# Performance work log

Measured on AMD Instinct MI355X. Metric: run time of the kernel, lower is better.

Reference implementation:

```python
import jax, jax.numpy as jnp
import numpy as np
import math

B, N, H, D = 2, 2048, 16, 64
NUM_BUCKETS, MAX_DIST = 32, 128
MODEL = H * D


def _rel_pos_bucket(rel, num_buckets, max_distance):
    # T5-style bucketing (bidirectional): half the buckets for sign, half log-spaced.
    nb = num_buckets // 2
    ret = (rel >= 0).astype(jnp.int32) * nb
    n = jnp.abs(rel)
    max_exact = nb // 2
    is_small = n < max_exact
    n_safe = jnp.maximum(n, 1).astype(jnp.float32)
    val_large = max_exact + (
        jnp.log(n_safe / max_exact) / math.log(max_distance / max_exact) * (nb - max_exact)
    ).astype(jnp.int32)
    val_large = jnp.minimum(val_large, nb - 1)
    return ret + jnp.where(is_small, n, val_large)


def _rel_pos_bias(rel_emb, n, m):
    q_pos = jnp.arange(m - n, m)
    k_pos = jnp.arange(m)
    rel = k_pos[None, :] - q_pos[:, None]            # [n, m]
    buckets = _rel_pos_bucket(rel, NUM_BUCKETS, MAX_DIST)
    bias = rel_emb[buckets]                          # [n, m, h]
    return bias.transpose(2, 0, 1)[None]             # [1, h, n, m]


def setup_inputs() -> dict:
    key = jax.random.key(0)
    ks = jax.random.split(key, 6)
    return {
        "q": jax.random.normal(ks[0], (B, N, MODEL), dtype=jnp.float32),
        "k": jax.random.normal(ks[1], (B, N, MODEL), dtype=jnp.float32),
        "v": jax.random.normal(ks[2], (B, N, MODEL), dtype=jnp.float32),
        "rel_emb": jax.random.normal(ks[3], (NUM_BUCKETS, H), dtype=jnp.float32) * 0.05,
        "w_out": jax.random.normal(ks[4], (MODEL, MODEL), dtype=jnp.float32) * (MODEL ** -0.5),
        "b_out": jax.random.normal(ks[5], (MODEL,), dtype=jnp.float32) * 0.02,
    }


def reference(q, k, v, rel_emb, w_out, b_out):
    b, n, _ = q.shape
    split = lambda x: x.reshape(b, n, H, D).transpose(0, 2, 1, 3)  # b h n d
    qh, kh, vh = split(q), split(k), split(v)
    sim = jnp.einsum('bhnd,bhmd->bhnm', qh, kh)
    sim = (sim + _rel_pos_bias(rel_emb, n, n)) * (D ** -0.5)  # note: scale AFTER bias, as in source
    attn = jax.nn.softmax(sim, axis=-1)
    out = jnp.einsum('bhnm,bhmd->bhnd', attn, vh)
    out = out.transpose(0, 2, 1, 3).reshape(b, n, H * D)
    return out @ w_out.T + b_out
```

## Files before the change

### kernel.cpp

```cpp
#include <hip/hip_runtime.h>

#define BB 2
#define NN 2048
#define HH 16
#define MODEL 1024
#define CSC 0.18033688011112042f

typedef short bf16x8 __attribute__((ext_vector_type(8)));
typedef float f32x4 __attribute__((ext_vector_type(4)));
typedef int i32x2 __attribute__((ext_vector_type(2)));

__device__ __forceinline__ unsigned short f2bf(float x) {
  unsigned int u = __builtin_bit_cast(unsigned int, x);
  u += 0x7fffu + ((u >> 16) & 1u);
  return (unsigned short)(u >> 16);
}

__device__ __forceinline__ unsigned int pack_bf2(float a, float b) {
  unsigned int ua = __builtin_bit_cast(unsigned int, a) + 0x8000u;
  unsigned int ub = __builtin_bit_cast(unsigned int, b) + 0x8000u;
  return __builtin_amdgcn_perm(ub, ua, 0x07060302u);
}

__device__ __forceinline__ float fast_exp2(float x) {
#if __has_builtin(__builtin_amdgcn_exp2f)
  return __builtin_amdgcn_exp2f(x);
#else
  return exp2f(x);
#endif
}

__device__ __forceinline__ f32x4 mfma16(bf16x8 a, bf16x8 b, f32x4 c) {
  return __builtin_amdgcn_mfma_f32_16x16x32_bf16(a, b, c, 0, 0, 0);
}

__device__ __forceinline__ void async_copy16(void* lds_base, const void* g) {
  __builtin_amdgcn_global_load_lds(
      (const __attribute__((address_space(1))) void*)g,
      (__attribute__((address_space(3))) void*)lds_base, 16, 0, 0);
}

__global__ void prep_kernel(const float* __restrict__ q, const float* __restrict__ k,
                            const float* __restrict__ w, const float* __restrict__ v,
                            const float* __restrict__ rel_emb,
                            unsigned short* __restrict__ qb, unsigned short* __restrict__ kb,
                            unsigned short* __restrict__ wb, unsigned short* __restrict__ vt,
                            float* __restrict__ biasTab) {
  __shared__ unsigned short tile[64][65];
  const int NQ4 = BB * NN * MODEL / 4;
  const int blk = blockIdx.x;
  if (blk < 9216) {
    int i = blk * 256 + threadIdx.x;
    const float* src;
    unsigned short* dst;
    int j = i;
    if (i < NQ4) {
      src = q; dst = qb;
    } else if (i < 2 * NQ4) {
      src = k; dst = kb; j = i - NQ4;
    } else {
      src = w; dst = wb; j = i - 2 * NQ4;
    }
    float4 f = reinterpret_cast<const float4*>(src)[j];
    ushort4 u;
    u.x = f2bf(f.x); u.y = f2bf(f.y); u.z = f2bf(f.z); u.w = f2bf(f.w);
    reinterpret_cast<ushort4*>(dst)[j] = u;
  } else if (blk < 10240) {
    const int blk2 = blk - 9216;
    const int n0 = (blk2 & 31) * 64;
    const int bh = blk2 >> 5;
    const int b = bh >> 4, h = bh & 15;
    const int c = threadIdx.x & 63;
    const int r = threadIdx.x >> 6;
#pragma unroll
    for (int i = 0; i < 16; ++i) {
      int nl = r * 16 + i;
      tile[c][nl] = f2bf(v[((long)(b * NN + n0 + nl)) * MODEL + h * 64 + c]);
    }
    __syncthreads();
#pragma unroll
    for (int i = 0; i < 16; ++i) {
      int d = r * 16 + i;
      vt[((long)(bh * 64 + d)) * NN + n0 + c] = tile[d][c];
    }
  } else {
    int idx = (blk - 10240) * 256 + threadIdx.x;
    if (idx >= 4095) return;
    int rel = idx - 2047;
    int nn = rel < 0 ? -rel : rel;
    int bucket;
    if (nn < 8) {
      bucket = nn;
    } else {
      float val = logf((float)nn * 0.125f) / logf(16.0f) * 8.0f;
      int vl = 8 + (int)val;
      if (vl > 15) vl = 15;
      bucket = vl;
    }
    if (rel >= 0) bucket += 16;
#pragma unroll
    for (int h = 0; h < 16; ++h)
      biasTab[h * 4095 + idx] = rel_emb[bucket * 16 + h] * CSC - 12.0f;
  }
}

__global__ __launch_bounds__(256, 2) void flash10(
    const unsigned short* __restrict__ qb, const unsigned short* __restrict__ kb,
    const unsigned short* __restrict__ vtb, const float* __restrict__ biasTab,
    unsigned short* __restrict__ attn) {
  __shared__ __align__(16) float obuf[4 * 64 * 68];
  __shared__ __align__(16) float scratch[512];

  const int i = blockIdx.x;
  const int bh = (i & 7) * 4 + ((i >> 3) >> 5);
  const int qt = (i >> 3) & 31;
  const int b = bh >> 4, h = bh & 15;
  const int q0 = qt * 64;
  const int tid = threadIdx.x, w = tid >> 6, lane = tid & 63;
  const int g = lane >> 4, c = lane & 15;

  const float* btab = biasTab + h * 4095 + 2047;
  for (int j = tid; j < 441; j += 256) scratch[j] = btab[j - 220];
  const float cPos = btab[200], cNeg = btab[-200];
  __syncthreads();

  bf16x8 qf0[4], qf1[4];
  const unsigned short* qbase = qb + ((long)(b * NN + q0)) * MODEL + h * 64;
#pragma unroll
  for (int nt = 0; nt < 4; ++nt) {
    const unsigned short* r = qbase + (16 * nt + c) * MODEL + 8 * g;
    qf0[nt] = *reinterpret_cast<const bf16x8*>(r);
    qf1[nt] = *reinterpret_cast<const bf16x8*>(r + 32);
  }

  const unsigned short* kbase = kb + ((long)b * NN) * MODEL + h * 64;
  const unsigned short* vbase = vtb + ((long)bh * 64) * NN;

  f32x4 o[4][4];
  float l_p[4] = {0.f, 0.f, 0.f, 0.f};
#pragma unroll
  for (int mt = 0; mt < 4; ++mt)
#pragma unroll
    for (int nt = 0; nt < 4; ++nt) o[mt][nt] = f32x4{0.f, 0.f, 0.f, 0.f};

  for (int it = 0; it < 8; ++it) {
    const int kt = w + 4 * it;
    bf16x8 kf0[4], kf1[4];
    const unsigned short* krow = kbase + (long)(kt * 64) * MODEL;
#pragma unroll
    for (int mt = 0; mt < 4; ++mt) {
      const unsigned short* r = krow + (16 * mt + c) * MODEL + 8 * g;
      kf0[mt] = *reinterpret_cast<const bf16x8*>(r);
      kf1[mt] = *reinterpret_cast<const bf16x8*>(r + 32);
    }
    bf16x8 vf0[4], vf1[4];
    const unsigned short* vrow = vbase + kt * 64;
#pragma unroll
    for (int mt = 0; mt < 4; ++mt) {
      const unsigned short* r = vrow + (long)(16 * mt + c) * NN + 8 * g;
      vf0[mt] = *reinterpret_cast<const bf16x8*>(r);
      vf1[mt] = *reinterpret_cast<const bf16x8*>(r + 32);
    }
    const int lo = kt * 64 - q0 - 63, hi = kt * 64 + 63 - q0;
    const bool sat = (lo >= 91 || hi <= -91);
    const float cb = (lo >= 91) ? cPos : cNeg;

#pragma unroll
    for (int nt = 0; nt < 4; ++nt) {
      f32x4 s[4];
#pragma unroll
      for (int mt = 0; mt < 4; ++mt) {
        s[mt] = mfma16(kf0[mt], qf0[nt], f32x4{0.f, 0.f, 0.f, 0.f});
        s[mt] = mfma16(kf1[mt], qf1[nt], s[mt]);
      }
      if (sat) {
#pragma unroll
        for (int mt = 0; mt < 4; ++mt)
#pragma unroll
          for (int rr = 0; rr < 4; ++rr) s[mt][rr] = s[mt][rr] * CSC + cb;
      } else {
        const int base = kt * 64 + 4 * g - q0 - 16 * nt - c + 220;
#pragma unroll
        for (int mt = 0; mt < 4; ++mt)
#pragma unroll
          for (int rr = 0; rr < 4; ++rr)
            s[mt][rr] = s[mt][rr] * CSC + scratch[base + 16 * mt + rr];
      }
      float sum = 0.f;
      unsigned int pk[4][2];
#pragma unroll
      for (int mt = 0; mt < 4; ++mt) {
        const float p0 = fast_exp2(s[mt][0]);
        const float p1 = fast_exp2(s[mt][1]);
        const float p2 = fast_exp2(s[mt][2]);
        const float p3 = fast_exp2(s[mt][3]);
        sum += (p0 + p1) + (p2 + p3);
        pk[mt][0] = pack_bf2(p0, p1);
        pk[mt][1] = pack_bf2(p2, p3);
      }
      l_p[nt] += sum;
      unsigned int d0, d1, d2, d3, d4, d5, d6, d7;
      {
        i32x2 x, y;
        x = __builtin_amdgcn_permlane32_swap((int)pk[0][0], (int)pk[1][0], false, false);
        y = __builtin_amdgcn_permlane16_swap(x[0], x[1], false, false);
        d0 = (unsigned int)y[0]; d2 = (unsigned int)y[1];
        x = __builtin_amdgcn_permlane32_swap((int)pk[0][1], (int)pk[1][1], false, false);
        y = __builtin_amdgcn_permlane16_swap(x[0], x[1], false, false);
        d1 = (unsigned int)y[0]; d3 = (unsigned int)y[1];
        x = __builtin_amdgcn_permlane32_swap((int)pk[2][0], (int)pk[3][0], false, false);
        y = __builtin_amdgcn_permlane16_swap(x[0], x[1], false, false);
        d4 = (unsigned int)y[0]; d6 = (unsigned int)y[1];
        x = __builtin_amdgcn_permlane32_swap((int)pk[2][1], (int)pk[3][1], false, false);
        y = __builtin_amdgcn_permlane16_swap(x[0], x[1], false, false);
        d5 = (unsigned int)y[0]; d7 = (unsigned int)y[1];
      }
      const bf16x8 pb0 = __builtin_bit_cast(bf16x8, uint4{d0, d1, d2, d3});
      const bf16x8 pb1 = __builtin_bit_cast(bf16x8, uint4{d4, d5, d6, d7});
#pragma unroll
      for (int mt = 0; mt < 4; ++mt) {
        o[mt][nt] = mfma16(vf0[mt], pb0, o[mt][nt]);
        o[mt][nt] = mfma16(vf1[mt], pb1, o[mt][nt]);
      }
    }
  }

  __syncthreads();
  float* ob = obuf + w * 64 * 68;
#pragma unroll
  for (int nt = 0; nt < 4; ++nt) {
    ob[(16 * nt + c) * 68 + 64 + g] = l_p[nt];
#pragma unroll
    for (int mt = 0; mt < 4; ++mt)
      *reinterpret_cast<f32x4*>(&ob[(16 * nt + c) * 68 + 16 * mt + 4 * g]) = o[mt][nt];
  }
  __syncthreads();

  const int qr = 16 * w + c;
  float l = 0.f;
#pragma unroll
  for (int u = 0; u < 4; ++u)
#pragma unroll
    for (int gg = 0; gg < 4; ++gg) l += obuf[(u * 64 + qr) * 68 + 64 + gg];
  const float inv = 1.f / l;

  float acc[16];
#pragma unroll
  for (int j = 0; j < 16; ++j) acc[j] = 0.f;
#pragma unroll
  for (int u = 0; u < 4; ++u) {
    const float* src = obuf + (u * 64 + qr) * 68;
    f32x4 r0 = *reinterpret_cast<const f32x4*>(&src[8 * g]);
    f32x4 r1 = *reinterpret_cast<const f32x4*>(&src[8 * g + 4]);
    f32x4 r2 = *reinterpret_cast<const f32x4*>(&src[32 + 8 * g]);
    f32x4 r3 = *reinterpret_cast<const f32x4*>(&src[32 + 8 * g + 4]);
#pragma unroll
    for (int j = 0; j < 4; ++j) {
      acc[j] += r0[j];
      acc[4 + j] += r1[j];
      acc[8 + j] += r2[j];
      acc[12 + j] += r3[j];
    }
  }
  unsigned int od[8];
#pragma unroll
  for (int t = 0; t < 8; ++t) od[t] = pack_bf2(acc[2 * t] * inv, acc[2 * t + 1] * inv);
  unsigned short* orow = attn + ((long)(b * NN + q0 + qr)) * MODEL + h * 64;
  *reinterpret_cast<uint4*>(orow + 8 * g) = uint4{od[0], od[1], od[2], od[3]};
  *reinterpret_cast<uint4*>(orow + 32 + 8 * g) = uint4{od[4], od[5], od[6], od[7]};
}

__global__ void proj_gemm_kernel(const unsigned short* __restrict__ A,
                                 const unsigned short* __restrict__ Bw,
                                 const float* __restrict__ bias,
                                 float* __restrict__ out) {
  __shared__ __align__(16) unsigned short At[2][128 * 64];
  __shared__ __align__(16) unsigned short Bt[2][64 * 64];
  int bm0 = blockIdx.x * 128, bn0 = blockIdx.y * 64;
  int tid = threadIdx.x, w = tid >> 6, lane = tid & 63;
  int g = lane >> 4, c = lane & 15;
  int m0 = (w & 1) * 64, n0 = (w >> 1) * 32;

  f32x4 acc[4][2];
#pragma unroll
  for (int mi = 0; mi < 4; ++mi)
#pragma unroll
    for (int nj = 0; nj < 2; ++nj) acc[mi][nj] = f32x4{0.f, 0.f, 0.f, 0.f};

  int rloc = lane >> 3, p = lane & 7;

  auto stage = [&](int buf, int kt) {
#pragma unroll
    for (int t = 0; t < 4; ++t) {
      int row = w * 32 + t * 8 + rloc;
      async_copy16(&At[buf][(w * 32 + t * 8) * 64],
                   A + (long)(bm0 + row) * 1024 + kt * 64 + (p ^ rloc) * 8);
    }
#pragma unroll
    for (int t = 0; t < 2; ++t) {
      int row = w * 16 + t * 8 + rloc;
      async_copy16(&Bt[buf][(w * 16 + t * 8) * 64],
                   Bw + (long)(bn0 + row) * 1024 + kt * 64 + (p ^ rloc) * 8);
    }
  };

  int cur = 0;
  stage(0, 0);
  for (int kt = 0; kt < 16; ++kt) {
    __syncthreads();
    if (kt < 15) stage(cur ^ 1, kt + 1);

    bf16x8 af0[4], af1[4], bf0[2], bf1[2];
#pragma unroll
    for (int mi = 0; mi < 4; ++mi) {
      int row = m0 + 16 * mi + c, sw = row & 7;
      af0[mi] = *reinterpret_cast<const bf16x8*>(&At[cur][row * 64 + (g ^ sw) * 8]);
      af1[mi] = *reinterpret_cast<const bf16x8*>(&At[cur][row * 64 + ((4 + g) ^ sw) * 8]);
    }
#pragma unroll
    for (int nj = 0; nj < 2; ++nj) {
      int row = n0 + 16 * nj + c, sw = row & 7;
      bf0[nj] = *reinterpret_cast<const bf16x8*>(&Bt[cur][row * 64 + (g ^ sw) * 8]);
      bf1[nj] = *reinterpret_cast<const bf16x8*>(&Bt[cur][row * 64 + ((4 + g) ^ sw) * 8]);
    }
#pragma unroll
    for (int mi = 0; mi < 4; ++mi)
#pragma unroll
      for (int nj = 0; nj < 2; ++nj) {
        acc[mi][nj] = mfma16(af0[mi], bf0[nj], acc[mi][nj]);
        acc[mi][nj] = mfma16(af1[mi], bf1[nj], acc[mi][nj]);
      }
    cur ^= 1;
  }

#pragma unroll
  for (int mi = 0; mi < 4; ++mi)
#pragma unroll
    for (int nj = 0; nj < 2; ++nj)
#pragma unroll
      for (int r = 0; r < 4; ++r) {
        int row = bm0 + m0 + mi * 16 + 4 * g + r;
        int col = bn0 + n0 + nj * 16 + c;
        out[(long)row * 1024 + col] = acc[mi][nj][r] + bias[col];
      }
}

extern "C" void kernel_launch(void* const* d_in, const int* in_sizes, int n_in,
                              void* d_out, int out_size, void* d_ws, size_t ws_size,
                              hipStream_t stream) {
  const float* q = (const float*)d_in[0];
  const float* k = (const float*)d_in[1];
  const float* v = (const float*)d_in[2];
  const float* rel_emb = (const float*)d_in[3];
  const float* w_out = (const float*)d_in[4];
  const float* b_out = (const float*)d_in[5];
  float* out = (float*)d_out;

  char* ws = (char*)d_ws;
  unsigned short* qb   = (unsigned short*)(ws);
  unsigned short* kb   = (unsigned short*)(ws + (8u << 20));
  unsigned short* vt   = (unsigned short*)(ws + (16u << 20));
  unsigned short* attn = (unsigned short*)(ws + (24u << 20));
  unsigned short* wb   = (unsigned short*)(ws + (32u << 20));
  float* biasTab       = (float*)(ws + (34u << 20));

  hipLaunchKernelGGL(prep_kernel, dim3(10257), dim3(256), 0, stream,
                     q, k, w_out, v, rel_emb, qb, kb, wb, vt, biasTab);
  hipLaunchKernelGGL(flash10, dim3(1024), dim3(256), 0, stream,
                     qb, kb, vt, biasTab, attn);
  hipLaunchKernelGGL(proj_gemm_kernel, dim3(32, 16), dim3(256), 0, stream,
                     attn, wb, b_out, out);
}
```

Before: 190.5 us.

## Fuse Q conversion into attention, double-buffer K loads, raise MFMA priority

Q is no longer converted to bf16 in the prep kernel. The attention kernel now reads fp32 Q directly and rounds it to bf16 in registers, which removes a full write and re-read of Q through global memory. The key-tile loop is manually unrolled with two register buffers so the next K tile is fetched while the current one is processed. s_setprio is raised around the MFMA groups to favour matrix issue. These add register pressure under the 2-blocks-per-CU launch bounds, and the Q fragment loads become twice as large.

```diff
diff --git a/kernel.cpp b/kernel.cpp
--- a/kernel.cpp
+++ b/kernel.cpp
@@ -20,6 +20,10 @@
   unsigned int ua = __builtin_bit_cast(unsigned int, a) + 0x8000u;
   unsigned int ub = __builtin_bit_cast(unsigned int, b) + 0x8000u;
   return __builtin_amdgcn_perm(ub, ua, 0x07060302u);
+}
+
+__device__ __forceinline__ unsigned int pack2_rne(float a, float b) {
+  return (unsigned int)f2bf(a) | ((unsigned int)f2bf(b) << 16);
 }
 
 __device__ __forceinline__ float fast_exp2(float x) {
@@ -40,33 +44,29 @@
       (__attribute__((address_space(3))) void*)lds_base, 16, 0, 0);
 }
 
-__global__ void prep_kernel(const float* __restrict__ q, const float* __restrict__ k,
-                            const float* __restrict__ w, const float* __restrict__ v,
-                            const float* __restrict__ rel_emb,
-                            unsigned short* __restrict__ qb, unsigned short* __restrict__ kb,
-                            unsigned short* __restrict__ wb, unsigned short* __restrict__ vt,
-                            float* __restrict__ biasTab) {
+__global__ void prep_kernel(const float* __restrict__ k, const float* __restrict__ w,
+                            const float* __restrict__ v, const float* __restrict__ rel_emb,
+                            unsigned short* __restrict__ kb, unsigned short* __restrict__ wb,
+                            unsigned short* __restrict__ vt, float* __restrict__ biasTab) {
   __shared__ unsigned short tile[64][65];
-  const int NQ4 = BB * NN * MODEL / 4;
+  const int NK4 = BB * NN * MODEL / 4;
   const int blk = blockIdx.x;
-  if (blk < 9216) {
+  if (blk < 5120) {
     int i = blk * 256 + threadIdx.x;
     const float* src;
     unsigned short* dst;
     int j = i;
-    if (i < NQ4) {
-      src = q; dst = qb;
-    } else if (i < 2 * NQ4) {
-      src = k; dst = kb; j = i - NQ4;
+    if (i < NK4) {
+      src = k; dst = kb;
     } else {
-      src = w; dst = wb; j = i - 2 * NQ4;
+      src = w; dst = wb; j = i - NK4;
     }
     float4 f = reinterpret_cast<const float4*>(src)[j];
     ushort4 u;
     u.x = f2bf(f.x); u.y = f2bf(f.y); u.z = f2bf(f.z); u.w = f2bf(f.w);
     reinterpret_cast<ushort4*>(dst)[j] = u;
-  } else if (blk < 10240) {
-    const int blk2 = blk - 9216;
+  } else if (blk < 6144) {
+    const int blk2 = blk - 5120;
     const int n0 = (blk2 & 31) * 64;
     const int bh = blk2 >> 5;
     const int b = bh >> 4, h = bh & 15;
@@ -84,7 +84,7 @@
       vt[((long)(bh * 64 + d)) * NN + n0 + c] = tile[d][c];
     }
   } else {
-    int idx = (blk - 10240) * 256 + threadIdx.x;
+    int idx = (blk - 6144) * 256 + threadIdx.x;
     if (idx >= 4095) return;
     int rel = idx - 2047;
     int nn = rel < 0 ? -rel : rel;
@@ -104,8 +104,8 @@
   }
 }
 
-__global__ __launch_bounds__(256, 2) void flash10(
-    const unsigned short* __restrict__ qb, const unsigned short* __restrict__ kb,
+__global__ __launch_bounds__(256, 2) void flash12(
+    const float* __restrict__ qf32, const unsigned short* __restrict__ kb,
     const unsigned short* __restrict__ vtb, const float* __restrict__ biasTab,
     unsigned short* __restrict__ attn) {
   __shared__ __align__(16) float obuf[4 * 64 * 68];
@@ -125,12 +125,18 @@
   __syncthreads();
 
   bf16x8 qf0[4], qf1[4];
-  const unsigned short* qbase = qb + ((long)(b * NN + q0)) * MODEL + h * 64;
+  const float* qbase = qf32 + ((long)(b * NN + q0)) * MODEL + h * 64;
 #pragma unroll
   for (int nt = 0; nt < 4; ++nt) {
-    const unsigned short* r = qbase + (16 * nt + c) * MODEL + 8 * g;
-    qf0[nt] = *reinterpret_cast<const bf16x8*>(r);
-    qf1[nt] = *reinterpret_cast<const bf16x8*>(r + 32);
+    const float* r = qbase + (16 * nt + c) * MODEL + 8 * g;
+    float4 f0 = *reinterpret_cast<const float4*>(r);
+    float4 f1 = *reinterpret_cast<const float4*>(r + 4);
+    float4 f2 = *reinterpret_cast<const float4*>(r + 32);
+    float4 f3 = *reinterpret_cast<const float4*>(r + 36);
+    qf0[nt] = __builtin_bit_cast(bf16x8, uint4{pack2_rne(f0.x, f0.y), pack2_rne(f0.z, f0.w),
+                                               pack2_rne(f1.x, f1.y), pack2_rne(f1.z, f1.w)});
+    qf1[nt] = __builtin_bit_cast(bf16x8, uint4{pack2_rne(f2.x, f2.y), pack2_rne(f2.z, f2.w),
+                                               pack2_rne(f3.x, f3.y), pack2_rne(f3.z, f3.w)});
   }
 
   const unsigned short* kbase = kb + ((long)b * NN) * MODEL + h * 64;
@@ -143,16 +149,19 @@
 #pragma unroll
     for (int nt = 0; nt < 4; ++nt) o[mt][nt] = f32x4{0.f, 0.f, 0.f, 0.f};
 
-  for (int it = 0; it < 8; ++it) {
-    const int kt = w + 4 * it;
-    bf16x8 kf0[4], kf1[4];
+  auto loadK = [&](int kt, bf16x8 (&K0)[4], bf16x8 (&K1)[4]) {
     const unsigned short* krow = kbase + (long)(kt * 64) * MODEL;
 #pragma unroll
     for (int mt = 0; mt < 4; ++mt) {
       const unsigned short* r = krow + (16 * mt + c) * MODEL + 8 * g;
-      kf0[mt] = *reinterpret_cast<const bf16x8*>(r);
-      kf1[mt] = *reinterpret_cast<const bf16x8*>(r + 32);
-    }
+      K0[mt] = *reinterpret_cast<const bf16x8*>(r);
+      K1[mt] = *reinterpret_cast<const bf16x8*>(r + 32);
+    }
+  };
+
+  auto body = [&](int it, bf16x8 (&K0)[4], bf16x8 (&K1)[4],
+                  bf16x8 (&N0)[4], bf16x8 (&N1)[4]) {
+    const int kt = w + 4 * it;
     bf16x8 vf0[4], vf1[4];
     const unsigned short* vrow = vbase + kt * 64;
 #pragma unroll
@@ -161,6 +170,8 @@
       vf0[mt] = *reinterpret_cast<const bf16x8*>(r);
       vf1[mt] = *reinterpret_cast<const bf16x8*>(r + 32);
     }
+    if (it < 7) loadK(kt + 4, N0, N1);
+
     const int lo = kt * 64 - q0 - 63, hi = kt * 64 + 63 - q0;
     const bool sat = (lo >= 91 || hi <= -91);
     const float cb = (lo >= 91) ? cPos : cNeg;
@@ -168,11 +179,13 @@
 #pragma unroll
     for (int nt = 0; nt < 4; ++nt) {
       f32x4 s[4];
+      __builtin_amdgcn_s_setprio(1);
 #pragma unroll
       for (int mt = 0; mt < 4; ++mt) {
-        s[mt] = mfma16(kf0[mt], qf0[nt], f32x4{0.f, 0.f, 0.f, 0.f});
-        s[mt] = mfma16(kf1[mt], qf1[nt], s[mt]);
-      }
+        s[mt] = mfma16(K0[mt], qf0[nt], f32x4{0.f, 0.f, 0.f, 0.f});
+        s[mt] = mfma16(K1[mt], qf1[nt], s[mt]);
+      }
+      __builtin_amdgcn_s_setprio(0);
       if (sat) {
 #pragma unroll
         for (int mt = 0; mt < 4; ++mt)
@@ -217,13 +230,26 @@
       }
       const bf16x8 pb0 = __builtin_bit_cast(bf16x8, uint4{d0, d1, d2, d3});
       const bf16x8 pb1 = __builtin_bit_cast(bf16x8, uint4{d4, d5, d6, d7});
+      __builtin_amdgcn_s_setprio(1);
 #pragma unroll
       for (int mt = 0; mt < 4; ++mt) {
         o[mt][nt] = mfma16(vf0[mt], pb0, o[mt][nt]);
         o[mt][nt] = mfma16(vf1[mt], pb1, o[mt][nt]);
       }
-    }
-  }
+      __builtin_amdgcn_s_setprio(0);
+    }
+  };
+
+  bf16x8 kA0[4], kA1[4], kB0[4], kB1[4];
+  loadK(w, kA0, kA1);
+  body(0, kA0, kA1, kB0, kB1);
+  body(1, kB0, kB1, kA0, kA1);
+  body(2, kA0, kA1, kB0, kB1);
+  body(3, kB0, kB1, kA0, kA1);
+  body(4, kA0, kA1, kB0, kB1);
+  body(5, kB0, kB1, kA0, kA1);
+  body(6, kA0, kA1, kB0, kB1);
+  body(7, kB0, kB1, kA0, kA1);
 
   __syncthreads();
   float* ob = obuf + w * 64 * 68;
@@ -357,17 +383,16 @@
   float* out = (float*)d_out;
 
   char* ws = (char*)d_ws;
-  unsigned short* qb   = (unsigned short*)(ws);
   unsigned short* kb   = (unsigned short*)(ws + (8u << 20));
   unsigned short* vt   = (unsigned short*)(ws + (16u << 20));
   unsigned short* attn = (unsigned short*)(ws + (24u << 20));
   unsigned short* wb   = (unsigned short*)(ws + (32u << 20));
   float* biasTab       = (float*)(ws + (34u << 20));
 
-  hipLaunchKernelGGL(prep_kernel, dim3(10257), dim3(256), 0, stream,
-                     q, k, w_out, v, rel_emb, qb, kb, wb, vt, biasTab);
-  hipLaunchKernelGGL(flash10, dim3(1024), dim3(256), 0, stream,
-                     qb, kb, vt, biasTab, attn);
+  hipLaunchKernelGGL(prep_kernel, dim3(6161), dim3(256), 0, stream,
+                     k, w_out, v, rel_emb, kb, wb, vt, biasTab);
+  hipLaunchKernelGGL(flash12, dim3(1024), dim3(256), 0, stream,
+                     q, kb, vt, biasTab, attn);
   hipLaunchKernelGGL(proj_gemm_kernel, dim3(32, 16), dim3(256), 0, stream,
                      attn, wb, b_out, out);
 }
```

Result: slower. 439.0 us (+130.5%).
